# Performance work log

Measured on AMD Instinct MI355X. Metric: run time of the kernel, lower is better.

The kernel has to match this reference:

```python
import jax, jax.numpy as jnp
import numpy as np

D_IN = 1024
D_OUT = 1024
NUM_HEADS = 16
HEAD_DIM = D_OUT // NUM_HEADS


def setup_inputs() -> dict:
    key = jax.random.key(0)
    ks = jax.random.split(key, 6)
    s = 0.02
    return {
        "x": jax.random.normal(ks[0], (4, 2048, D_IN), dtype=jnp.float32),
        "W_q": jax.random.normal(ks[1], (D_IN, D_OUT), dtype=jnp.float32) * s,
        "W_k": jax.random.normal(ks[2], (D_IN, D_OUT), dtype=jnp.float32) * s,
        "W_v": jax.random.normal(ks[3], (D_IN, D_OUT), dtype=jnp.float32) * s,
        "W_o": jax.random.normal(ks[4], (D_OUT, D_OUT), dtype=jnp.float32) * s,
        "b_o": jax.random.normal(ks[5], (D_OUT,), dtype=jnp.float32) * s,
    }


def reference(x, W_q, W_k, W_v, W_o, b_o):
    b, n, _ = x.shape
    # project and split heads: [b, h, n, d]
    q = (x @ W_q).reshape(b, n, NUM_HEADS, HEAD_DIM).transpose(0, 2, 1, 3)
    k = (x @ W_k).reshape(b, n, NUM_HEADS, HEAD_DIM).transpose(0, 2, 1, 3)
    v = (x @ W_v).reshape(b, n, NUM_HEADS, HEAD_DIM).transpose(0, 2, 1, 3)
    scores = jnp.einsum("bhqd,bhkd->bhqk", q, k)
    causal = jnp.tril(jnp.ones((n, n), dtype=bool))  # True = keep
    scores = jnp.where(causal, scores, -jnp.inf)
    attn = jax.nn.softmax(scores / np.sqrt(HEAD_DIM).astype(np.float32), axis=-1)
    ctx = jnp.einsum("bhqk,bhkd->bhqd", attn, v)
    ctx = ctx.transpose(0, 2, 1, 3).reshape(b, n, D_OUT)
    return ctx @ W_o + b_o
```

## Files before the change

kernel.cpp:

```cpp
#include <hip/hip_runtime.h>
#include <hip/hip_bf16.h>

#define NHEADS 16
#define HDIM 64
#define SEQ 2048
#define BATCH 4
#define DMODEL 1024
#define MTOT (BATCH * SEQ)

typedef short v8s __attribute__((ext_vector_type(8)));
typedef short v4s __attribute__((ext_vector_type(4)));
typedef float v4f __attribute__((ext_vector_type(4)));
typedef unsigned short u16;
typedef unsigned int u32;

__device__ __forceinline__ u16 f2bf(float f) {
    union { float f; unsigned u; } v; v.f = f;
    unsigned r = v.u + 0x7FFFu + ((v.u >> 16) & 1u);
    return (u16)(r >> 16);
}
__device__ __forceinline__ u16 f2bf_fast(float f) {
    union { float f; unsigned u; } v; v.f = f;
    return (u16)((v.u + 0x8000u) >> 16);
}

__device__ __forceinline__ void g2l16(const u16* g, short* l) {
    __builtin_amdgcn_global_load_lds(
        (const __attribute__((address_space(1))) u32*)g,
        (__attribute__((address_space(3))) u32*)l, 16, 0, 0);
}

__global__ __launch_bounds__(256)
void xcvt(const float* __restrict__ x, u16* __restrict__ xb)
{
    size_t i = ((size_t)blockIdx.x * 256 + threadIdx.x) * 8;
    v4f a = *(const v4f*)&x[i];
    v4f b = *(const v4f*)&x[i + 4];
    v8s p;
#pragma unroll
    for (int e = 0; e < 4; ++e) p[e] = (short)f2bf(a[e]);
#pragma unroll
    for (int e = 0; e < 4; ++e) p[4 + e] = (short)f2bf(b[e]);
    *(v8s*)&xb[i] = p;
}

__global__ __launch_bounds__(256)
void transpose_w(const float* __restrict__ src, u16* __restrict__ dst)
{
    __shared__ __align__(8) short Ts[64 * 68];
    const int k0 = blockIdx.x * 64, n0 = blockIdx.y * 64;
    const int t = threadIdx.x;
    const int n4 = (t & 15) * 4, kl = t >> 4;
#pragma unroll
    for (int it = 0; it < 4; ++it) {
        int k = kl + 16 * it;
        v4f v = *(const v4f*)&src[(size_t)(k0 + k) * DMODEL + n0 + n4];
        v4s p;
#pragma unroll
        for (int e = 0; e < 4; ++e) p[e] = (short)f2bf(v[e]);
        *(v4s*)&Ts[k * 68 + n4] = p;
    }
    __syncthreads();
    const int nl = t >> 4, k4 = (t & 15) * 4;
#pragma unroll
    for (int it = 0; it < 4; ++it) {
        int n = nl + 16 * it;
        v4s o;
#pragma unroll
        for (int e = 0; e < 4; ++e) o[e] = Ts[(k4 + e) * 68 + n];
        *(v4s*)&dst[(size_t)(n0 + n) * DMODEL + k0 + k4] = o;
    }
}

#define QSCALE (0.125f * 1.44269504088896f)

__device__ __forceinline__ void qkv_epilogue(
    v4f (&acc)[4][4], int which, int n0, int m0, int wn, int wm,
    int l15, int quad, u16* Qb, u16* Kb, u16* Vt)
{
    if (which == 2) {
#pragma unroll
        for (int i = 0; i < 4; ++i)
#pragma unroll
            for (int j = 0; j < 4; ++j) {
                int col = n0 + wn + j * 16 + l15;
                int h = col >> 6, d = col & 63;
                int m = m0 + wm + i * 16 + quad * 4;
                int b = m >> 11, n = m & (SEQ - 1);
                v4s pv;
#pragma unroll
                for (int r = 0; r < 4; ++r) pv[r] = (short)f2bf(acc[i][j][r]);
                *(v4s*)&Vt[((size_t)(b * NHEADS + h) * HDIM + d) * SEQ + n] = pv;
            }
    } else {
        u16* Ob = (which == 0) ? Qb : Kb;
        const float scale = (which == 0) ? QSCALE : 1.0f;
#pragma unroll
        for (int i = 0; i < 4; ++i)
#pragma unroll
            for (int j = 0; j < 4; ++j) {
                int col = n0 + wn + j * 16 + l15;
                int h = col >> 6, d = col & 63;
#pragma unroll
                for (int r = 0; r < 4; ++r) {
                    int m = m0 + wm + i * 16 + quad * 4 + r;
                    int b = m >> 11, n = m & (SEQ - 1);
                    Ob[((size_t)(b * NHEADS + h) * SEQ + n) * HDIM + d] =
                        f2bf(acc[i][j][r] * scale);
                }
            }
    }
}

__global__ __launch_bounds__(256, 2)
void qkv_fast(const u16* __restrict__ xb, const u16* __restrict__ Wt,
              u16* __restrict__ Qb, u16* __restrict__ Kb, u16* __restrict__ Vt)
{
    __shared__ __align__(16) short As[128 * 32];
    __shared__ __align__(16) short Bs[128 * 32];

    const int which = blockIdx.z;
    const u16* W = Wt + (size_t)which * DMODEL * DMODEL;

    const int n0 = blockIdx.x * 128;
    const int m0 = blockIdx.y * 128;
    const int t = threadIdx.x;
    const int lane = t & 63;
    const int l15 = lane & 15;
    const int quad = lane >> 4;
    const int wave = t >> 6;
    const int wm = (wave >> 1) * 64;
    const int wn = (wave & 1) * 64;
    const int srow = t >> 2;
    const int sc8 = (t & 3) * 8;

    v4f acc[4][4];
#pragma unroll
    for (int i = 0; i < 4; ++i)
#pragma unroll
        for (int j = 0; j < 4; ++j) acc[i][j] = {0.f, 0.f, 0.f, 0.f};

    for (int k0 = 0; k0 < DMODEL; k0 += 32) {
        __syncthreads();
        g2l16(&xb[(size_t)(m0 + srow) * DMODEL + k0 + sc8], &As[srow * 32 + sc8]);
        g2l16(&xb[(size_t)(m0 + 64 + srow) * DMODEL + k0 + sc8],
              &As[(64 + srow) * 32 + sc8]);
        g2l16(&W[(size_t)(n0 + srow) * DMODEL + k0 + sc8], &Bs[srow * 32 + sc8]);
        g2l16(&W[(size_t)(n0 + 64 + srow) * DMODEL + k0 + sc8],
              &Bs[(64 + srow) * 32 + sc8]);
        __syncthreads();

        v8s af[4], bf[4];
#pragma unroll
        for (int i = 0; i < 4; ++i)
            af[i] = *(const v8s*)&As[(wm + i * 16 + l15) * 32 + quad * 8];
#pragma unroll
        for (int j = 0; j < 4; ++j)
            bf[j] = *(const v8s*)&Bs[(wn + j * 16 + l15) * 32 + quad * 8];
#pragma unroll
        for (int i = 0; i < 4; ++i)
#pragma unroll
            for (int j = 0; j < 4; ++j)
                acc[i][j] = __builtin_amdgcn_mfma_f32_16x16x32_bf16(
                    af[i], bf[j], acc[i][j], 0, 0, 0);
    }
    qkv_epilogue(acc, which, n0, m0, wn, wm, l15, quad, Qb, Kb, Vt);
}

__global__ __launch_bounds__(256, 2)
void qkv_slow(const float* __restrict__ x, const u16* __restrict__ Wt,
              u16* __restrict__ Qb, u16* __restrict__ Kb, u16* __restrict__ Vt)
{
    __shared__ __align__(16) short As[128 * 32];
    __shared__ __align__(16) short Bs[128 * 32];

    const int which = blockIdx.z;
    const u16* W = Wt + (size_t)which * DMODEL * DMODEL;

    const int n0 = blockIdx.x * 128;
    const int m0 = blockIdx.y * 128;
    const int t = threadIdx.x;
    const int lane = t & 63;
    const int l15 = lane & 15;
    const int quad = lane >> 4;
    const int wave = t >> 6;
    const int wm = (wave >> 1) * 64;
    const int wn = (wave & 1) * 64;
    const int srow = t >> 2;
    const int sc8 = (t & 3) * 8;

    v4f acc[4][4];
#pragma unroll
    for (int i = 0; i < 4; ++i)
#pragma unroll
        for (int j = 0; j < 4; ++j) acc[i][j] = {0.f, 0.f, 0.f, 0.f};

    for (int k0 = 0; k0 < DMODEL; k0 += 32) {
        __syncthreads();
        g2l16(&W[(size_t)(n0 + srow) * DMODEL + k0 + sc8], &Bs[srow * 32 + sc8]);
        g2l16(&W[(size_t)(n0 + 64 + srow) * DMODEL + k0 + sc8],
              &Bs[(64 + srow) * 32 + sc8]);
#pragma unroll
        for (int it = 0; it < 2; ++it) {
            int row = srow + 64 * it;
            const float* xp = &x[(size_t)(m0 + row) * DMODEL + k0 + sc8];
            v4f x0 = *(const v4f*)xp;
            v4f x1 = *(const v4f*)(xp + 4);
            v8s av;
#pragma unroll
            for (int e = 0; e < 4; ++e) av[e] = (short)f2bf(x0[e]);
#pragma unroll
            for (int e = 0; e < 4; ++e) av[4 + e] = (short)f2bf(x1[e]);
            *(v8s*)&As[row * 32 + sc8] = av;
        }
        __syncthreads();

        v8s af[4], bf[4];
#pragma unroll
        for (int i = 0; i < 4; ++i)
            af[i] = *(const v8s*)&As[(wm + i * 16 + l15) * 32 + quad * 8];
#pragma unroll
        for (int j = 0; j < 4; ++j)
            bf[j] = *(const v8s*)&Bs[(wn + j * 16 + l15) * 32 + quad * 8];
#pragma unroll
        for (int i = 0; i < 4; ++i)
#pragma unroll
            for (int j = 0; j < 4; ++j)
                acc[i][j] = __builtin_amdgcn_mfma_f32_16x16x32_bf16(
                    af[i], bf[j], acc[i][j], 0, 0, 0);
    }
    qkv_epilogue(acc, which, n0, m0, wn, wm, l15, quad, Qb, Kb, Vt);
}

#define KP 72

__global__ __launch_bounds__(256, 4)
void attn(const u16* __restrict__ Qb, const u16* __restrict__ Kb,
          const u16* __restrict__ Vt, u16* __restrict__ Cx)
{
    __shared__ __align__(16) short Ks[64 * KP];
    __shared__ __align__(16) short Vs[64 * KP];
    __shared__ __align__(16) short Ps[4 * 16 * KP];

    const int ell = blockIdx.x;
    const int xcd = ell & 7;
    const int rest = ell >> 3;
    const int p = rest & 15;
    const int bh = ((rest >> 4) << 3) | xcd;

    const int t = threadIdx.x;
    const int lane = t & 63;
    const int l15 = lane & 15;
    const int quad = lane >> 4;
    const int wave = t >> 6;

    const u16* Qh = Qb + (size_t)bh * SEQ * HDIM;
    const u16* Kh = Kb + (size_t)bh * SEQ * HDIM;
    const u16* Vh = Vt + (size_t)bh * HDIM * SEQ;
    short* Pw = &Ps[wave * 16 * KP];

    const int skey = t >> 2;
    const int sd = (t & 3) * 16;
    const int b = bh >> 4, h = bh & 15;

#pragma unroll 1
    for (int phase = 0; phase < 2; ++phase) {
        const int qt = phase ? p : (31 - p);
        const int q0w = qt * 64 + wave * 16;

        v8s qf[2];
#pragma unroll
        for (int hh = 0; hh < 2; ++hh)
            qf[hh] = *(const v8s*)
                &Qh[(size_t)(q0w + l15) * HDIM + hh * 32 + quad * 8];

        v4f o[4];
        float ls[4];
#pragma unroll
        for (int j = 0; j < 4; ++j) o[j] = {0.f, 0.f, 0.f, 0.f};
#pragma unroll
        for (int r = 0; r < 4; ++r) ls[r] = 0.f;

        v8s pk0, pk1, pv0, pv1;
        {
            const u16* Kp = &Kh[(size_t)skey * HDIM + sd];
            pk0 = *(const v8s*)Kp; pk1 = *(const v8s*)(Kp + 8);
            const u16* Vp = &Vh[(size_t)skey * SEQ + sd];
            pv0 = *(const v8s*)Vp; pv1 = *(const v8s*)(Vp + 8);
        }

#pragma unroll 1
        for (int kb = 0; kb <= qt; ++kb) {
            __syncthreads();
            *(v8s*)&Ks[skey * KP + sd] = pk0;
            *(v8s*)&Ks[skey * KP + sd + 8] = pk1;
            *(v8s*)&Vs[skey * KP + sd] = pv0;
            *(v8s*)&Vs[skey * KP + sd + 8] = pv1;
            __syncthreads();

            if (kb < qt) {
                const u16* Kp = &Kh[(size_t)((kb + 1) * 64 + skey) * HDIM + sd];
                pk0 = *(const v8s*)Kp; pk1 = *(const v8s*)(Kp + 8);
                const u16* Vp = &Vh[(size_t)skey * SEQ + (kb + 1) * 64 + sd];
                pv0 = *(const v8s*)Vp; pv1 = *(const v8s*)(Vp + 8);
            }

            const bool tail = (kb == qt);
#pragma unroll
            for (int s = 0; s < 4; ++s) {
                v8s kf0 = *(const v8s*)&Ks[(s * 16 + l15) * KP + quad * 8];
                v8s kf1 = *(const v8s*)&Ks[(s * 16 + l15) * KP + 32 + quad * 8];
                v4f a = {0.f, 0.f, 0.f, 0.f};
                a = __builtin_amdgcn_mfma_f32_16x16x32_bf16(qf[0], kf0, a, 0, 0, 0);
                a = __builtin_amdgcn_mfma_f32_16x16x32_bf16(qf[1], kf1, a, 0, 0, 0);
                int key = kb * 64 + s * 16 + l15;
#pragma unroll
                for (int r = 0; r < 4; ++r) {
                    int qrow = q0w + quad * 4 + r;
                    float pe = (tail && key > qrow) ? 0.f : exp2f(a[r]);
                    ls[r] += pe;
                    Pw[(quad * 4 + r) * KP + s * 16 + l15] = (short)f2bf_fast(pe);
                }
            }
            __asm__ volatile("s_waitcnt lgkmcnt(0)" ::: "memory");
#pragma unroll
            for (int ks = 0; ks < 2; ++ks) {
                v8s pa = *(const v8s*)&Pw[l15 * KP + ks * 32 + quad * 8];
#pragma unroll
                for (int j = 0; j < 4; ++j) {
                    v8s vf = *(const v8s*)
                        &Vs[(j * 16 + l15) * KP + ks * 32 + quad * 8];
                    o[j] = __builtin_amdgcn_mfma_f32_16x16x32_bf16(
                        pa, vf, o[j], 0, 0, 0);
                }
            }
        }

#pragma unroll
        for (int r = 0; r < 4; ++r) {
            float v = ls[r];
            v += __shfl_xor(v, 1, 64);
            v += __shfl_xor(v, 2, 64);
            v += __shfl_xor(v, 4, 64);
            v += __shfl_xor(v, 8, 64);
            ls[r] = 1.f / v;
        }
#pragma unroll
        for (int j = 0; j < 4; ++j)
#pragma unroll
            for (int r = 0; r < 4; ++r) {
                int qrow = q0w + quad * 4 + r;
                Cx[((size_t)(b * SEQ + qrow)) * DMODEL + h * HDIM + j * 16 + l15]
                    = f2bf(o[j][r] * ls[r]);
            }
    }
}

__global__ __launch_bounds__(256, 2)
void out_gemm(const u16* __restrict__ Cx, const u16* __restrict__ WoT,
              const float* __restrict__ bo, float* __restrict__ Y)
{
    __shared__ __align__(16) short As[128 * 32];
    __shared__ __align__(16) short Bs[128 * 32];

    const int n0 = blockIdx.x * 128;
    const int m0 = blockIdx.y * 128;
    const int t = threadIdx.x;
    const int lane = t & 63;
    const int l15 = lane & 15;
    const int quad = lane >> 4;
    const int wave = t >> 6;
    const int wm = (wave >> 1) * 64;
    const int wn = (wave & 1) * 64;
    const int srow = t >> 2;
    const int sc8 = (t & 3) * 8;

    v4f acc[4][4];
#pragma unroll
    for (int i = 0; i < 4; ++i)
#pragma unroll
        for (int j = 0; j < 4; ++j) acc[i][j] = {0.f, 0.f, 0.f, 0.f};

    for (int k0 = 0; k0 < DMODEL; k0 += 32) {
        __syncthreads();
        g2l16(&Cx[(size_t)(m0 + srow) * DMODEL + k0 + sc8], &As[srow * 32 + sc8]);
        g2l16(&Cx[(size_t)(m0 + 64 + srow) * DMODEL + k0 + sc8],
              &As[(64 + srow) * 32 + sc8]);
        g2l16(&WoT[(size_t)(n0 + srow) * DMODEL + k0 + sc8], &Bs[srow * 32 + sc8]);
        g2l16(&WoT[(size_t)(n0 + 64 + srow) * DMODEL + k0 + sc8],
              &Bs[(64 + srow) * 32 + sc8]);
        __syncthreads();

        v8s af[4], bf[4];
#pragma unroll
        for (int i = 0; i < 4; ++i)
            af[i] = *(const v8s*)&As[(wm + i * 16 + l15) * 32 + quad * 8];
#pragma unroll
        for (int j = 0; j < 4; ++j)
            bf[j] = *(const v8s*)&Bs[(wn + j * 16 + l15) * 32 + quad * 8];
#pragma unroll
        for (int i = 0; i < 4; ++i)
#pragma unroll
            for (int j = 0; j < 4; ++j)
                acc[i][j] = __builtin_amdgcn_mfma_f32_16x16x32_bf16(
                    af[i], bf[j], acc[i][j], 0, 0, 0);
    }

#pragma unroll
    for (int i = 0; i < 4; ++i)
#pragma unroll
        for (int j = 0; j < 4; ++j) {
            int col = n0 + wn + j * 16 + l15;
            float bias = bo[col];
#pragma unroll
            for (int r = 0; r < 4; ++r) {
                int m = m0 + wm + i * 16 + quad * 4 + r;
                Y[(size_t)m * DMODEL + col] = acc[i][j][r] + bias;
            }
        }
}

extern "C" void kernel_launch(void* const* d_in, const int* in_sizes, int n_in,
                              void* d_out, int out_size, void* d_ws,
                              size_t ws_size, hipStream_t stream)
{
    const float* x  = (const float*)d_in[0];
    const float* Wq = (const float*)d_in[1];
    const float* Wk = (const float*)d_in[2];
    const float* Wv = (const float*)d_in[3];
    const float* Wo = (const float*)d_in[4];
    const float* bo = (const float*)d_in[5];
    float* Y = (float*)d_out;

    const size_t per = (size_t)BATCH * NHEADS * SEQ * HDIM;
    const size_t wsz = (size_t)DMODEL * DMODEL;
    u16* base = (u16*)d_ws;

    if (ws_size >= (size_t)72 * 1024 * 1024) {
        u16* xb  = base;
        u16* Cx  = base;
        u16* Wt4 = base + per;
        u16* Qb  = base + per + 4 * wsz;
        u16* Kb  = Qb + per;
        u16* Vt  = Kb + per;

        xcvt<<<MTOT * DMODEL / (256 * 8), 256, 0, stream>>>(x, xb);
        transpose_w<<<dim3(16, 16), 256, 0, stream>>>(Wq, Wt4);
        transpose_w<<<dim3(16, 16), 256, 0, stream>>>(Wk, Wt4 + wsz);
        transpose_w<<<dim3(16, 16), 256, 0, stream>>>(Wv, Wt4 + 2 * wsz);
        transpose_w<<<dim3(16, 16), 256, 0, stream>>>(Wo, Wt4 + 3 * wsz);
        qkv_fast<<<dim3(DMODEL / 128, MTOT / 128, 3), 256, 0, stream>>>(
            xb, Wt4, Qb, Kb, Vt);
        attn<<<1024, 256, 0, stream>>>(Qb, Kb, Vt, Cx);
        out_gemm<<<dim3(DMODEL / 128, MTOT / 128), 256, 0, stream>>>(
            Cx, Wt4 + 3 * wsz, bo, Y);
    } else {
        u16* Wt  = base;
        u16* Cx  = base;
        u16* Qb  = base + per;
        u16* WoT = base + per;
        u16* Kb  = base + 2 * per;
        u16* Vt  = base + 3 * per;

        transpose_w<<<dim3(16, 16), 256, 0, stream>>>(Wq, Wt);
        transpose_w<<<dim3(16, 16), 256, 0, stream>>>(Wk, Wt + wsz);
        transpose_w<<<dim3(16, 16), 256, 0, stream>>>(Wv, Wt + 2 * wsz);
        qkv_slow<<<dim3(DMODEL / 128, MTOT / 128, 3), 256, 0, stream>>>(
            x, Wt, Qb, Kb, Vt);
        attn<<<1024, 256, 0, stream>>>(Qb, Kb, Vt, Cx);
        transpose_w<<<dim3(16, 16), 256, 0, stream>>>(Wo, WoT);
        out_gemm<<<dim3(DMODEL / 128, MTOT / 128), 256, 0, stream>>>(
            Cx, WoT, bo, Y);
    }
}
```

Measured before the change: 288.7 us.

## Double GEMM K-tile, batch weight transposes, split causal mask branch in attention

The QKV and output GEMMs now stage 64-wide K tiles instead of 32, halving the number of barrier-separated load/compute iterations. The four weight transposes are merged into one launch using a z grid dimension. In attention, the mask check runs only on the diagonal block through a separate branch, and the P scratch buffer gets a wider padded stride (88) to change LDS bank mapping. Doubling the LDS tiles increases shared memory per block, which may lower occupancy.

```diff
diff --git a/kernel.cpp b/kernel.cpp
--- a/kernel.cpp
+++ b/kernel.cpp
@@ -44,11 +44,10 @@
     *(v8s*)&xb[i] = p;
 }
 
-__global__ __launch_bounds__(256)
-void transpose_w(const float* __restrict__ src, u16* __restrict__ dst)
+__device__ __forceinline__ void transpose_body(
+    const float* __restrict__ src, u16* __restrict__ dst, int k0, int n0)
 {
     __shared__ __align__(8) short Ts[64 * 68];
-    const int k0 = blockIdx.x * 64, n0 = blockIdx.y * 64;
     const int t = threadIdx.x;
     const int n4 = (t & 15) * 4, kl = t >> 4;
 #pragma unroll
@@ -70,6 +69,23 @@
         for (int e = 0; e < 4; ++e) o[e] = Ts[(k4 + e) * 68 + n];
         *(v4s*)&dst[(size_t)(n0 + n) * DMODEL + k0 + k4] = o;
     }
+}
+
+__global__ __launch_bounds__(256)
+void transpose_w(const float* __restrict__ src, u16* __restrict__ dst)
+{
+    transpose_body(src, dst, blockIdx.x * 64, blockIdx.y * 64);
+}
+
+__global__ __launch_bounds__(256)
+void transpose_w4(const float* __restrict__ s0, const float* __restrict__ s1,
+                  const float* __restrict__ s2, const float* __restrict__ s3,
+                  u16* __restrict__ dst)
+{
+    const int z = blockIdx.z;
+    const float* src = (z == 0) ? s0 : (z == 1) ? s1 : (z == 2) ? s2 : s3;
+    transpose_body(src, dst + (size_t)z * DMODEL * DMODEL,
+                   blockIdx.x * 64, blockIdx.y * 64);
 }
 
 #define QSCALE (0.125f * 1.44269504088896f)
@@ -114,6 +130,67 @@
 
 __global__ __launch_bounds__(256, 2)
 void qkv_fast(const u16* __restrict__ xb, const u16* __restrict__ Wt,
+              u16* __restrict__ Qb, u16* __restrict__ Kb, u16* __restrict__ Vt)
+{
+    __shared__ __align__(16) short As[128 * 64];
+    __shared__ __align__(16) short Bs[128 * 64];
+
+    const int which = blockIdx.z;
+    const u16* W = Wt + (size_t)which * DMODEL * DMODEL;
+
+    const int n0 = blockIdx.x * 128;
+    const int m0 = blockIdx.y * 128;
+    const int t = threadIdx.x;
+    const int lane = t & 63;
+    const int l15 = lane & 15;
+    const int quad = lane >> 4;
+    const int wave = t >> 6;
+    const int wm = (wave >> 1) * 64;
+    const int wn = (wave & 1) * 64;
+    const int srow = t >> 3;
+    const int sc8 = (t & 7) * 8;
+
+    v4f acc[4][4];
+#pragma unroll
+    for (int i = 0; i < 4; ++i)
+#pragma unroll
+        for (int j = 0; j < 4; ++j) acc[i][j] = {0.f, 0.f, 0.f, 0.f};
+
+    for (int k0 = 0; k0 < DMODEL; k0 += 64) {
+        __syncthreads();
+#pragma unroll
+        for (int c = 0; c < 4; ++c) {
+            g2l16(&xb[(size_t)(m0 + c * 32 + srow) * DMODEL + k0 + sc8],
+                  &As[(c * 32 + srow) * 64 + sc8]);
+            g2l16(&W[(size_t)(n0 + c * 32 + srow) * DMODEL + k0 + sc8],
+                  &Bs[(c * 32 + srow) * 64 + sc8]);
+        }
+        __syncthreads();
+
+#pragma unroll
+        for (int kh = 0; kh < 2; ++kh) {
+            v8s af[4], bf[4];
+#pragma unroll
+            for (int i = 0; i < 4; ++i)
+                af[i] = *(const v8s*)
+                    &As[(wm + i * 16 + l15) * 64 + kh * 32 + quad * 8];
+#pragma unroll
+            for (int j = 0; j < 4; ++j)
+                bf[j] = *(const v8s*)
+                    &Bs[(wn + j * 16 + l15) * 64 + kh * 32 + quad * 8];
+#pragma unroll
+            for (int i = 0; i < 4; ++i)
+#pragma unroll
+                for (int j = 0; j < 4; ++j)
+                    acc[i][j] = __builtin_amdgcn_mfma_f32_16x16x32_bf16(
+                        af[i], bf[j], acc[i][j], 0, 0, 0);
+        }
+    }
+    qkv_epilogue(acc, which, n0, m0, wn, wm, l15, quad, Qb, Kb, Vt);
+}
+
+__global__ __launch_bounds__(256, 2)
+void qkv_slow(const float* __restrict__ x, const u16* __restrict__ Wt,
               u16* __restrict__ Qb, u16* __restrict__ Kb, u16* __restrict__ Vt)
 {
     __shared__ __align__(16) short As[128 * 32];
@@ -142,12 +219,22 @@
 
     for (int k0 = 0; k0 < DMODEL; k0 += 32) {
         __syncthreads();
-        g2l16(&xb[(size_t)(m0 + srow) * DMODEL + k0 + sc8], &As[srow * 32 + sc8]);
-        g2l16(&xb[(size_t)(m0 + 64 + srow) * DMODEL + k0 + sc8],
-              &As[(64 + srow) * 32 + sc8]);
         g2l16(&W[(size_t)(n0 + srow) * DMODEL + k0 + sc8], &Bs[srow * 32 + sc8]);
         g2l16(&W[(size_t)(n0 + 64 + srow) * DMODEL + k0 + sc8],
               &Bs[(64 + srow) * 32 + sc8]);
+#pragma unroll
+        for (int it = 0; it < 2; ++it) {
+            int row = srow + 64 * it;
+            const float* xp = &x[(size_t)(m0 + row) * DMODEL + k0 + sc8];
+            v4f x0 = *(const v4f*)xp;
+            v4f x1 = *(const v4f*)(xp + 4);
+            v8s av;
+#pragma unroll
+            for (int e = 0; e < 4; ++e) av[e] = (short)f2bf(x0[e]);
+#pragma unroll
+            for (int e = 0; e < 4; ++e) av[4 + e] = (short)f2bf(x1[e]);
+            *(v8s*)&As[row * 32 + sc8] = av;
+        }
         __syncthreads();
 
         v8s af[4], bf[4];
@@ -167,15 +254,161 @@
     qkv_epilogue(acc, which, n0, m0, wn, wm, l15, quad, Qb, Kb, Vt);
 }
 
+#define KP 72
+#define PP 88
+
+__global__ __launch_bounds__(256, 4)
+void attn(const u16* __restrict__ Qb, const u16* __restrict__ Kb,
+          const u16* __restrict__ Vt, u16* __restrict__ Cx)
+{
+    __shared__ __align__(16) short Ks[64 * KP];
+    __shared__ __align__(16) short Vs[64 * KP];
+    __shared__ __align__(16) short Ps[4 * 16 * PP];
+
+    const int ell = blockIdx.x;
+    const int xcd = ell & 7;
+    const int rest = ell >> 3;
+    const int p = rest & 15;
+    const int bh = ((rest >> 4) << 3) | xcd;
+
+    const int t = threadIdx.x;
+    const int lane = t & 63;
+    const int l15 = lane & 15;
+    const int quad = lane >> 4;
+    const int wave = t >> 6;
+
+    const u16* Qh = Qb + (size_t)bh * SEQ * HDIM;
+    const u16* Kh = Kb + (size_t)bh * SEQ * HDIM;
+    const u16* Vh = Vt + (size_t)bh * HDIM * SEQ;
+    short* Pw = &Ps[wave * 16 * PP];
+
+    const int skey = t >> 2;
+    const int sd = (t & 3) * 16;
+    const int b = bh >> 4, h = bh & 15;
+
+#pragma unroll 1
+    for (int phase = 0; phase < 2; ++phase) {
+        const int qt = phase ? p : (31 - p);
+        const int q0w = qt * 64 + wave * 16;
+
+        v8s qf[2];
+#pragma unroll
+        for (int hh = 0; hh < 2; ++hh)
+            qf[hh] = *(const v8s*)
+                &Qh[(size_t)(q0w + l15) * HDIM + hh * 32 + quad * 8];
+
+        v4f o[4];
+        float ls[4];
+#pragma unroll
+        for (int j = 0; j < 4; ++j) o[j] = {0.f, 0.f, 0.f, 0.f};
+#pragma unroll
+        for (int r = 0; r < 4; ++r) ls[r] = 0.f;
+
+        v8s pk0, pk1, pv0, pv1;
+        {
+            const u16* Kp = &Kh[(size_t)skey * HDIM + sd];
+            pk0 = *(const v8s*)Kp; pk1 = *(const v8s*)(Kp + 8);
+            const u16* Vp = &Vh[(size_t)skey * SEQ + sd];
+            pv0 = *(const v8s*)Vp; pv1 = *(const v8s*)(Vp + 8);
+        }
+
+#pragma unroll 1
+        for (int kb = 0; kb <= qt; ++kb) {
+            __syncthreads();
+            *(v8s*)&Ks[skey * KP + sd] = pk0;
+            *(v8s*)&Ks[skey * KP + sd + 8] = pk1;
+            *(v8s*)&Vs[skey * KP + sd] = pv0;
+            *(v8s*)&Vs[skey * KP + sd + 8] = pv1;
+            __syncthreads();
+
+            if (kb < qt) {
+                const u16* Kp = &Kh[(size_t)((kb + 1) * 64 + skey) * HDIM + sd];
+                pk0 = *(const v8s*)Kp; pk1 = *(const v8s*)(Kp + 8);
+                const u16* Vp = &Vh[(size_t)skey * SEQ + (kb + 1) * 64 + sd];
+                pv0 = *(const v8s*)Vp; pv1 = *(const v8s*)(Vp + 8);
+            }
+
+            if (kb < qt) {
+#pragma unroll
+                for (int s = 0; s < 4; ++s) {
+                    v8s kf0 = *(const v8s*)&Ks[(s * 16 + l15) * KP + quad * 8];
+                    v8s kf1 = *(const v8s*)
+                        &Ks[(s * 16 + l15) * KP + 32 + quad * 8];
+                    v4f a = {0.f, 0.f, 0.f, 0.f};
+                    a = __builtin_amdgcn_mfma_f32_16x16x32_bf16(
+                        qf[0], kf0, a, 0, 0, 0);
+                    a = __builtin_amdgcn_mfma_f32_16x16x32_bf16(
+                        qf[1], kf1, a, 0, 0, 0);
+#pragma unroll
+                    for (int r = 0; r < 4; ++r) {
+                        float pe = exp2f(a[r]);
+                        ls[r] += pe;
+                        Pw[(quad * 4 + r) * PP + s * 16 + l15] =
+                            (short)f2bf_fast(pe);
+                    }
+                }
+            } else {
+#pragma unroll
+                for (int s = 0; s < 4; ++s) {
+                    v8s kf0 = *(const v8s*)&Ks[(s * 16 + l15) * KP + quad * 8];
+                    v8s kf1 = *(const v8s*)
+                        &Ks[(s * 16 + l15) * KP + 32 + quad * 8];
+                    v4f a = {0.f, 0.f, 0.f, 0.f};
+                    a = __builtin_amdgcn_mfma_f32_16x16x32_bf16(
+                        qf[0], kf0, a, 0, 0, 0);
+                    a = __builtin_amdgcn_mfma_f32_16x16x32_bf16(
+                        qf[1], kf1, a, 0, 0, 0);
+                    int key = kb * 64 + s * 16 + l15;
+#pragma unroll
+                    for (int r = 0; r < 4; ++r) {
+                        int qrow = q0w + quad * 4 + r;
+                        float pe = (key > qrow) ? 0.f : exp2f(a[r]);
+                        ls[r] += pe;
+                        Pw[(quad * 4 + r) * PP + s * 16 + l15] =
+                            (short)f2bf_fast(pe);
+                    }
+                }
+            }
+            __asm__ volatile("s_waitcnt lgkmcnt(0)" ::: "memory");
+#pragma unroll
+            for (int ks = 0; ks < 2; ++ks) {
+                v8s pa = *(const v8s*)&Pw[l15 * PP + ks * 32 + quad * 8];
+#pragma unroll
+                for (int j = 0; j < 4; ++j) {
+                    v8s vf = *(const v8s*)
+                        &Vs[(j * 16 + l15) * KP + ks * 32 + quad * 8];
+                    o[j] = __builtin_amdgcn_mfma_f32_16x16x32_bf16(
+                        pa, vf, o[j], 0, 0, 0);
+                }
+            }
+        }
+
+#pragma unroll
+        for (int r = 0; r < 4; ++r) {
+            float v = ls[r];
+            v += __shfl_xor(v, 1, 64);
+            v += __shfl_xor(v, 2, 64);
+            v += __shfl_xor(v, 4, 64);
+            v += __shfl_xor(v, 8, 64);
+            ls[r] = 1.f / v;
+        }
+#pragma unroll
+        for (int j = 0; j < 4; ++j)
+#pragma unroll
+            for (int r = 0; r < 4; ++r) {
+                int qrow = q0w + quad * 4 + r;
+                Cx[((size_t)(b * SEQ + qrow)) * DMODEL + h * HDIM + j * 16 + l15]
+                    = f2bf(o[j][r] * ls[r]);
+            }
+    }
+}
+
 __global__ __launch_bounds__(256, 2)
-void qkv_slow(const float* __restrict__ x, const u16* __restrict__ Wt,
-              u16* __restrict__ Qb, u16* __restrict__ Kb, u16* __restrict__ Vt)
-{
-    __shared__ __align__(16) short As[128 * 32];
-    __shared__ __align__(16) short Bs[128 * 32];
-
-    const int which = blockIdx.z;
-    const u16* W = Wt + (size_t)which * DMODEL * DMODEL;
+void out_gemm(const u16* __restrict__ Cx, const u16* __restrict__ WoT,
+              const float* __restrict__ bo, float* __restrict__ Y)
+{
+    __shared__ __align__(16) short As[128 * 64];
+    __shared__ __align__(16) short Bs[128 * 64];
 
     const int n0 = blockIdx.x * 128;
     const int m0 = blockIdx.y * 128;
@@ -186,8 +419,8 @@
     const int wave = t >> 6;
     const int wm = (wave >> 1) * 64;
     const int wn = (wave & 1) * 64;
-    const int srow = t >> 2;
-    const int sc8 = (t & 3) * 8;
+    const int srow = t >> 3;
+    const int sc8 = (t & 7) * 8;
 
     v4f acc[4][4];
 #pragma unroll
@@ -195,215 +428,35 @@
 #pragma unroll
         for (int j = 0; j < 4; ++j) acc[i][j] = {0.f, 0.f, 0.f, 0.f};
 
-    for (int k0 = 0; k0 < DMODEL; k0 += 32) {
+    for (int k0 = 0; k0 < DMODEL; k0 += 64) {
         __syncthreads();
-        g2l16(&W[(size_t)(n0 + srow) * DMODEL + k0 + sc8], &Bs[srow * 32 + sc8]);
-        g2l16(&W[(size_t)(n0 + 64 + srow) * DMODEL + k0 + sc8],
-              &Bs[(64 + srow) * 32 + sc8]);
-#pragma unroll
-        for (int it = 0; it < 2; ++it) {
-            int row = srow + 64 * it;
-            const float* xp = &x[(size_t)(m0 + row) * DMODEL + k0 + sc8];
-            v4f x0 = *(const v4f*)xp;
-            v4f x1 = *(const v4f*)(xp + 4);
-            v8s av;
-#pragma unroll
-            for (int e = 0; e < 4; ++e) av[e] = (short)f2bf(x0[e]);
-#pragma unroll
-            for (int e = 0; e < 4; ++e) av[4 + e] = (short)f2bf(x1[e]);
-            *(v8s*)&As[row * 32 + sc8] = av;
+#pragma unroll
+        for (int c = 0; c < 4; ++c) {
+            g2l16(&Cx[(size_t)(m0 + c * 32 + srow) * DMODEL + k0 + sc8],
+                  &As[(c * 32 + srow) * 64 + sc8]);
+            g2l16(&WoT[(size_t)(n0 + c * 32 + srow) * DMODEL + k0 + sc8],
+                  &Bs[(c * 32 + srow) * 64 + sc8]);
         }
         __syncthreads();
 
-        v8s af[4], bf[4];
-#pragma unroll
-        for (int i = 0; i < 4; ++i)
-            af[i] = *(const v8s*)&As[(wm + i * 16 + l15) * 32 + quad * 8];
-#pragma unroll
-        for (int j = 0; j < 4; ++j)
-            bf[j] = *(const v8s*)&Bs[(wn + j * 16 + l15) * 32 + quad * 8];
-#pragma unroll
-        for (int i = 0; i < 4; ++i)
+#pragma unroll
+        for (int kh = 0; kh < 2; ++kh) {
+            v8s af[4], bf[4];
+#pragma unroll
+            for (int i = 0; i < 4; ++i)
+                af[i] = *(const v8s*)
+                    &As[(wm + i * 16 + l15) * 64 + kh * 32 + quad * 8];
 #pragma unroll
             for (int j = 0; j < 4; ++j)
-                acc[i][j] = __builtin_amdgcn_mfma_f32_16x16x32_bf16(
-                    af[i], bf[j], acc[i][j], 0, 0, 0);
-    }
-    qkv_epilogue(acc, which, n0, m0, wn, wm, l15, quad, Qb, Kb, Vt);
-}
-
-#define KP 72
-
-__global__ __launch_bounds__(256, 4)
-void attn(const u16* __restrict__ Qb, const u16* __restrict__ Kb,
-          const u16* __restrict__ Vt, u16* __restrict__ Cx)
-{
-    __shared__ __align__(16) short Ks[64 * KP];
-    __shared__ __align__(16) short Vs[64 * KP];
-    __shared__ __align__(16) short Ps[4 * 16 * KP];
-
-    const int ell = blockIdx.x;
-    const int xcd = ell & 7;
-    const int rest = ell >> 3;
-    const int p = rest & 15;
-    const int bh = ((rest >> 4) << 3) | xcd;
-
-    const int t = threadIdx.x;
-    const int lane = t & 63;
-    const int l15 = lane & 15;
-    const int quad = lane >> 4;
-    const int wave = t >> 6;
-
-    const u16* Qh = Qb + (size_t)bh * SEQ * HDIM;
-    const u16* Kh = Kb + (size_t)bh * SEQ * HDIM;
-    const u16* Vh = Vt + (size_t)bh * HDIM * SEQ;
-    short* Pw = &Ps[wave * 16 * KP];
-
-    const int skey = t >> 2;
-    const int sd = (t & 3) * 16;
-    const int b = bh >> 4, h = bh & 15;
-
-#pragma unroll 1
-    for (int phase = 0; phase < 2; ++phase) {
-        const int qt = phase ? p : (31 - p);
-        const int q0w = qt * 64 + wave * 16;
-
-        v8s qf[2];
-#pragma unroll
-        for (int hh = 0; hh < 2; ++hh)
-            qf[hh] = *(const v8s*)
-                &Qh[(size_t)(q0w + l15) * HDIM + hh * 32 + quad * 8];
-
-        v4f o[4];
-        float ls[4];
-#pragma unroll
-        for (int j = 0; j < 4; ++j) o[j] = {0.f, 0.f, 0.f, 0.f};
-#pragma unroll
-        for (int r = 0; r < 4; ++r) ls[r] = 0.f;
-
-        v8s pk0, pk1, pv0, pv1;
-        {
-            const u16* Kp = &Kh[(size_t)skey * HDIM + sd];
-            pk0 = *(const v8s*)Kp; pk1 = *(const v8s*)(Kp + 8);
-            const u16* Vp = &Vh[(size_t)skey * SEQ + sd];
-            pv0 = *(const v8s*)Vp; pv1 = *(const v8s*)(Vp + 8);
-        }
-
-#pragma unroll 1
-        for (int kb = 0; kb <= qt; ++kb) {
-            __syncthreads();
-            *(v8s*)&Ks[skey * KP + sd] = pk0;
-            *(v8s*)&Ks[skey * KP + sd + 8] = pk1;
-            *(v8s*)&Vs[skey * KP + sd] = pv0;
-            *(v8s*)&Vs[skey * KP + sd + 8] = pv1;
-            __syncthreads();
-
-            if (kb < qt) {
-                const u16* Kp = &Kh[(size_t)((kb + 1) * 64 + skey) * HDIM + sd];
-                pk0 = *(const v8s*)Kp; pk1 = *(const v8s*)(Kp + 8);
-                const u16* Vp = &Vh[(size_t)skey * SEQ + (kb + 1) * 64 + sd];
-                pv0 = *(const v8s*)Vp; pv1 = *(const v8s*)(Vp + 8);
-            }
-
-            const bool tail = (kb == qt);
-#pragma unroll
-            for (int s = 0; s < 4; ++s) {
-                v8s kf0 = *(const v8s*)&Ks[(s * 16 + l15) * KP + quad * 8];
-                v8s kf1 = *(const v8s*)&Ks[(s * 16 + l15) * KP + 32 + quad * 8];
-                v4f a = {0.f, 0.f, 0.f, 0.f};
-                a = __builtin_amdgcn_mfma_f32_16x16x32_bf16(qf[0], kf0, a, 0, 0, 0);
-                a = __builtin_amdgcn_mfma_f32_16x16x32_bf16(qf[1], kf1, a, 0, 0, 0);
-                int key = kb * 64 + s * 16 + l15;
-#pragma unroll
-                for (int r = 0; r < 4; ++r) {
-                    int qrow = q0w + quad * 4 + r;
-                    float pe = (tail && key > qrow) ? 0.f : exp2f(a[r]);
-                    ls[r] += pe;
-                    Pw[(quad * 4 + r) * KP + s * 16 + l15] = (short)f2bf_fast(pe);
-                }
-            }
-            __asm__ volatile("s_waitcnt lgkmcnt(0)" ::: "memory");
-#pragma unroll
-            for (int ks = 0; ks < 2; ++ks) {
-                v8s pa = *(const v8s*)&Pw[l15 * KP + ks * 32 + quad * 8];
-#pragma unroll
-                for (int j = 0; j < 4; ++j) {
-                    v8s vf = *(const v8s*)
-                        &Vs[(j * 16 + l15) * KP + ks * 32 + quad * 8];
-                    o[j] = __builtin_amdgcn_mfma_f32_16x16x32_bf16(
-                        pa, vf, o[j], 0, 0, 0);
-                }
-            }
-        }
-
-#pragma unroll
-        for (int r = 0; r < 4; ++r) {
-            float v = ls[r];
-            v += __shfl_xor(v, 1, 64);
-            v += __shfl_xor(v, 2, 64);
-            v += __shfl_xor(v, 4, 64);
-            v += __shfl_xor(v, 8, 64);
-            ls[r] = 1.f / v;
-        }
-#pragma unroll
-        for (int j = 0; j < 4; ++j)
-#pragma unroll
-            for (int r = 0; r < 4; ++r) {
-                int qrow = q0w + quad * 4 + r;
-                Cx[((size_t)(b * SEQ + qrow)) * DMODEL + h * HDIM + j * 16 + l15]
-                    = f2bf(o[j][r] * ls[r]);
-            }
-    }
-}
-
-__global__ __launch_bounds__(256, 2)
-void out_gemm(const u16* __restrict__ Cx, const u16* __restrict__ WoT,
-              const float* __restrict__ bo, float* __restrict__ Y)
-{
-    __shared__ __align__(16) short As[128 * 32];
-    __shared__ __align__(16) short Bs[128 * 32];
-
-    const int n0 = blockIdx.x * 128;
-    const int m0 = blockIdx.y * 128;
-    const int t = threadIdx.x;
-    const int lane = t & 63;
-    const int l15 = lane & 15;
-    const int quad = lane >> 4;
-    const int wave = t >> 6;
-    const int wm = (wave >> 1) * 64;
-    const int wn = (wave & 1) * 64;
-    const int srow = t >> 2;
-    const int sc8 = (t & 3) * 8;
-
-    v4f acc[4][4];
-#pragma unroll
-    for (int i = 0; i < 4; ++i)
-#pragma unroll
-        for (int j = 0; j < 4; ++j) acc[i][j] = {0.f, 0.f, 0.f, 0.f};
-
-    for (int k0 = 0; k0 < DMODEL; k0 += 32) {
-        __syncthreads();
-        g2l16(&Cx[(size_t)(m0 + srow) * DMODEL + k0 + sc8], &As[srow * 32 + sc8]);
-        g2l16(&Cx[(size_t)(m0 + 64 + srow) * DMODEL + k0 + sc8],
-              &As[(64 + srow) * 32 + sc8]);
-        g2l16(&WoT[(size_t)(n0 + srow) * DMODEL + k0 + sc8], &Bs[srow * 32 + sc8]);
-        g2l16(&WoT[(size_t)(n0 + 64 + srow) * DMODEL + k0 + sc8],
-              &Bs[(64 + srow) * 32 + sc8]);
-        __syncthreads();
-
-        v8s af[4], bf[4];
-#pragma unroll
-        for (int i = 0; i < 4; ++i)
-            af[i] = *(const v8s*)&As[(wm + i * 16 + l15) * 32 + quad * 8];
-#pragma unroll
-        for (int j = 0; j < 4; ++j)
-            bf[j] = *(const v8s*)&Bs[(wn + j * 16 + l15) * 32 + quad * 8];
-#pragma unroll
-        for (int i = 0; i < 4; ++i)
-#pragma unroll
-            for (int j = 0; j < 4; ++j)
-                acc[i][j] = __builtin_amdgcn_mfma_f32_16x16x32_bf16(
-                    af[i], bf[j], acc[i][j], 0, 0, 0);
+                bf[j] = *(const v8s*)
+                    &Bs[(wn + j * 16 + l15) * 64 + kh * 32 + quad * 8];
+#pragma unroll
+            for (int i = 0; i < 4; ++i)
+#pragma unroll
+                for (int j = 0; j < 4; ++j)
+                    acc[i][j] = __builtin_amdgcn_mfma_f32_16x16x32_bf16(
+                        af[i], bf[j], acc[i][j], 0, 0, 0);
+        }
     }
 
 #pragma unroll
@@ -445,10 +498,7 @@
         u16* Vt  = Kb + per;
 
         xcvt<<<MTOT * DMODEL / (256 * 8), 256, 0, stream>>>(x, xb);
-        transpose_w<<<dim3(16, 16), 256, 0, stream>>>(Wq, Wt4);
-        transpose_w<<<dim3(16, 16), 256, 0, stream>>>(Wk, Wt4 + wsz);
-        transpose_w<<<dim3(16, 16), 256, 0, stream>>>(Wv, Wt4 + 2 * wsz);
-        transpose_w<<<dim3(16, 16), 256, 0, stream>>>(Wo, Wt4 + 3 * wsz);
+        transpose_w4<<<dim3(16, 16, 4), 256, 0, stream>>>(Wq, Wk, Wv, Wo, Wt4);
         qkv_fast<<<dim3(DMODEL / 128, MTOT / 128, 3), 256, 0, stream>>>(
             xb, Wt4, Qb, Kb, Vt);
         attn<<<1024, 256, 0, stream>>>(Qb, Kb, Vt, Cx);
```

Result: faster. 274.9 us (-4.8%).
